# Optimization experiments

Measured on AMD Instinct MI355X. Metric: run time of the kernel, lower is better.

## Reference

```python
import jax, jax.numpy as jnp
import numpy as np

B, TQ, TK, H = 8, 64, 8192, 256


def setup_inputs() -> dict:
    key = jax.random.key(0)
    k1, k2, k3, k4 = jax.random.split(key, 4)
    query = jax.random.normal(k1, (B, TQ, H), dtype=jnp.float32)
    keys = jax.random.normal(k2, (B, TK, H), dtype=jnp.float32)
    # nn.Linear(H, H): weight [H, H], bias [H]; scale like torch default-ish
    Wa_w = jax.random.normal(k3, (H, H), dtype=jnp.float32) * (1.0 / np.sqrt(H))
    Wa_b = jax.random.normal(k4, (H,), dtype=jnp.float32) * 0.01
    return {"query": query, "keys": keys, "Wa_w": Wa_w, "Wa_b": Wa_b}


def reference(query, keys, Wa_w, Wa_b):
    # keys_transformed = keys @ Wa_w.T + Wa_b  (torch Linear semantics)
    keys_t = jnp.einsum('bkh,oh->bko', keys, Wa_w) + Wa_b  # [B,TK,H]
    scores = jnp.einsum('bqh,bkh->bqk', query, keys_t)       # [B,TQ,TK]
    weights = jax.nn.softmax(scores, axis=-1)
    context = jnp.einsum('bqk,bkh->bqh', weights, keys)      # [B,TQ,H]
    return (context, weights)
```

## Files before the change

### kernel.cpp

```cpp
#include <hip/hip_runtime.h>

#define B 8
#define TQ 64
#define TK 8192
#define H 256

#define KSPLIT 32
#define KPB (TK / KSPLIT)
#define CRS 72

typedef __attribute__((ext_vector_type(8))) short bf16x8;
typedef __attribute__((ext_vector_type(4))) float f32x4;
typedef __attribute__((ext_vector_type(4))) unsigned short u16x4;
typedef __attribute__((ext_vector_type(2))) unsigned int u32x2;

static __device__ inline unsigned short f2bf_rne(float x) {
    unsigned int u = __float_as_uint(x);
    unsigned int r = (u + 0x7fffu + ((u >> 16) & 1u)) >> 16;
    return (unsigned short)r;
}

__global__ __launch_bounds__(256) void qtransform_kernel(
    const float* __restrict__ query, const float* __restrict__ Wa_w,
    const float* __restrict__ Wa_b, unsigned short* __restrict__ qthi,
    unsigned short* __restrict__ qtlo, float* __restrict__ qb)
{
    __shared__ float q_s[H];
    __shared__ float red[4];
    const int r = blockIdx.x;
    const int t = threadIdx.x;
    q_s[t] = query[r * H + t];
    __syncthreads();

    float a0 = 0.f, a1 = 0.f, a2 = 0.f, a3 = 0.f;
    for (int o = 0; o < H; o += 4) {
        a0 += q_s[o + 0] * Wa_w[(o + 0) * H + t];
        a1 += q_s[o + 1] * Wa_w[(o + 1) * H + t];
        a2 += q_s[o + 2] * Wa_w[(o + 2) * H + t];
        a3 += q_s[o + 3] * Wa_w[(o + 3) * H + t];
    }
    const float s = (a0 + a1) + (a2 + a3);
    const unsigned int u = __float_as_uint(s);
    const float hif = __uint_as_float(u & 0xFFFF0000u);
    const float lof = s - hif;
    qthi[r * H + t] = (unsigned short)(u >> 16);
    qtlo[r * H + t] = (unsigned short)(__float_as_uint(lof) >> 16);

    float p = q_s[t] * Wa_b[t];
    for (int off = 32; off > 0; off >>= 1) p += __shfl_down(p, off, 64);
    if ((t & 63) == 0) red[t >> 6] = p;
    __syncthreads();
    if (t == 0) qb[r] = (red[0] + red[1]) + (red[2] + red[3]);
}


#define STAGE1(v, row, khb) {                                                  \
    unsigned int u0=__float_as_uint(v.x), u1=__float_as_uint(v.y);             \
    unsigned int u2=__float_as_uint(v.z), u3=__float_as_uint(v.w);             \
    unsigned int h01=(u0>>16)|(u1&0xFFFF0000u), h23=(u2>>16)|(u3&0xFFFF0000u); \
    float l0=v.x-__uint_as_float(u0&0xFFFF0000u);                              \
    float l1=v.y-__uint_as_float(u1&0xFFFF0000u);                              \
    float l2=v.z-__uint_as_float(u2&0xFFFF0000u);                              \
    float l3=v.w-__uint_as_float(u3&0xFFFF0000u);                              \
    unsigned int q01=(__float_as_uint(l0)>>16)|(__float_as_uint(l1)&0xFFFF0000u); \
    unsigned int q23=(__float_as_uint(l2)>>16)|(__float_as_uint(l3)&0xFFFF0000u); \
    int bo=(row)*128 + (((hf>>1)^((row)&7))<<4) + ((hf&1)<<3);                 \
    *(u32x2*)((char*)b_hi+bo) = (u32x2){h01,h23};                              \
    *(u32x2*)((char*)b_lo+bo) = (u32x2){q01,q23};                              \
    *(u32x2*)&khb[(size_t)(row)*H + hf*4] = (u32x2){h01,h23}; }

#define LOADCHUNK(d0,d1,d2,d3, hc)                                             \
    d0 = *(const float4*)&kbase_g[(size_t)(sr +  0) * H + (hc) + hf * 4];      \
    d1 = *(const float4*)&kbase_g[(size_t)(sr + 16) * H + (hc) + hf * 4];      \
    d2 = *(const float4*)&kbase_g[(size_t)(sr + 32) * H + (hc) + hf * 4];      \
    d3 = *(const float4*)&kbase_g[(size_t)(sr + 48) * H + (hc) + hf * 4];

#define STAGECHUNK(v0,v1,v2,v3, hc) {                                          \
    unsigned short* khb = khi_ws + ((size_t)b * TK + k0g) * H + (hc);          \
    STAGE1(v0, sr +  0, khb); STAGE1(v1, sr + 16, khb);                        \
    STAGE1(v2, sr + 32, khb); STAGE1(v3, sr + 48, khb); }

#define COMPUTE(hc) {                                                          \
    _Pragma("unroll")                                                          \
    for (int hs = 0; hs < 64; hs += 32) {                                      \
        bf16x8 ah = *(const bf16x8*)&ah_base[(hc) + hs + lgrp * 8];            \
        bf16x8 al = *(const bf16x8*)&al_base[(hc) + hs + lgrp * 8];            \
        _Pragma("unroll")                                                      \
        for (int nt = 0; nt < 4; ++nt) {                                       \
            int rr = 16 * nt + lrow;                                           \
            int rb = rr * 128 + ((((hs >> 3) + lgrp) ^ (rr & 7)) << 4);        \
            bf16x8 bh = *(const bf16x8*)((const char*)b_hi + rb);              \
            bf16x8 bl = *(const bf16x8*)((const char*)b_lo + rb);              \
            acc[nt] = __builtin_amdgcn_mfma_f32_16x16x32_bf16(ah, bh, acc[nt], 0, 0, 0); \
            acc[nt] = __builtin_amdgcn_mfma_f32_16x16x32_bf16(ah, bl, acc[nt], 0, 0, 0); \
            acc[nt] = __builtin_amdgcn_mfma_f32_16x16x32_bf16(al, bh, acc[nt], 0, 0, 0); \
        } } }

__global__ __launch_bounds__(256, 4) void scores_kernel(
    const unsigned short* __restrict__ qthi, const unsigned short* __restrict__ qtlo,
    const float* __restrict__ qb, const float* __restrict__ keys,
    unsigned short* __restrict__ khi_ws, float* __restrict__ sraw,
    float* __restrict__ pm, float* __restrict__ ps)
{
    __shared__ unsigned short b_hi[64 * 64];
    __shared__ unsigned short b_lo[64 * 64];
    const int t    = threadIdx.x;
    const int kt   = blockIdx.x;
    const int b    = blockIdx.y;
    const int k0g  = kt * 64;
    const int w    = t >> 6;
    const int lane = t & 63;
    const int lrow = lane & 15;
    const int lgrp = lane >> 4;
    const int sr   = t >> 4;
    const int hf   = t & 15;

    const float* kbase_g = keys + (size_t)(b * TK + k0g) * H;
    const unsigned short* ah_base = qthi + (size_t)(b * TQ + 16 * w + lrow) * H;
    const unsigned short* al_base = qtlo + (size_t)(b * TQ + 16 * w + lrow) * H;

    f32x4 acc[4];
    #pragma unroll
    for (int nt = 0; nt < 4; ++nt) acc[nt] = (f32x4){0.f, 0.f, 0.f, 0.f};

    float4 r0, r1, r2, r3, p0, p1, p2, p3;
    LOADCHUNK(r0, r1, r2, r3, 0)

    LOADCHUNK(p0, p1, p2, p3, 64)
    STAGECHUNK(r0, r1, r2, r3, 0)
    __syncthreads();
    COMPUTE(0)
    __syncthreads();

    LOADCHUNK(r0, r1, r2, r3, 128)
    STAGECHUNK(p0, p1, p2, p3, 64)
    __syncthreads();
    COMPUTE(64)
    __syncthreads();

    LOADCHUNK(p0, p1, p2, p3, 192)
    STAGECHUNK(r0, r1, r2, r3, 128)
    __syncthreads();
    COMPUTE(128)
    __syncthreads();

    STAGECHUNK(p0, p1, p2, p3, 192)
    __syncthreads();
    COMPUTE(192)

    #pragma unroll
    for (int j = 0; j < 4; ++j) {
        const int qrow = 16 * w + lgrp * 4 + j;
        const float bias = qb[b * TQ + qrow];
        float v0 = acc[0][j] + bias, v1 = acc[1][j] + bias;
        float v2 = acc[2][j] + bias, v3 = acc[3][j] + bias;
        float* dst = &sraw[(size_t)(b * TQ + qrow) * TK + k0g + lrow];
        dst[0] = v0; dst[16] = v1; dst[32] = v2; dst[48] = v3;
        float m = fmaxf(fmaxf(v0, v1), fmaxf(v2, v3));
        m = fmaxf(m, __shfl_xor(m, 1, 64));
        m = fmaxf(m, __shfl_xor(m, 2, 64));
        m = fmaxf(m, __shfl_xor(m, 4, 64));
        m = fmaxf(m, __shfl_xor(m, 8, 64));
        float e = __expf(v0 - m) + __expf(v1 - m) + __expf(v2 - m) + __expf(v3 - m);
        e += __shfl_xor(e, 1, 64);
        e += __shfl_xor(e, 2, 64);
        e += __shfl_xor(e, 4, 64);
        e += __shfl_xor(e, 8, 64);
        if (lrow == 0) {
            pm[(size_t)(b * TQ + qrow) * 128 + kt] = m;
            ps[(size_t)(b * TQ + qrow) * 128 + kt] = e;
        }
    }
}

__global__ __launch_bounds__(128) void rowreduce_kernel(
    const float* __restrict__ pm, const float* __restrict__ ps,
    float* __restrict__ Mrow, float* __restrict__ Sinv)
{
    const int r = blockIdx.x;
    const int t = threadIdx.x;
    __shared__ float mred[2], sred[2];
    float m = pm[(size_t)r * 128 + t];
    for (int off = 32; off > 0; off >>= 1) m = fmaxf(m, __shfl_xor(m, off, 64));
    if ((t & 63) == 0) mred[t >> 6] = m;
    __syncthreads();
    const float M = fmaxf(mred[0], mred[1]);
    float s = ps[(size_t)r * 128 + t] * __expf(pm[(size_t)r * 128 + t] - M);
    for (int off = 32; off > 0; off >>= 1) s += __shfl_xor(s, off, 64);
    if ((t & 63) == 0) sred[t >> 6] = s;
    __syncthreads();
    if (t == 0) { Mrow[r] = M; Sinv[r] = 1.0f / (sred[0] + sred[1]); }
}

__global__ __launch_bounds__(256) void context_main_kernel(
    const float* __restrict__ sraw, const float* __restrict__ Mrow,
    const float* __restrict__ Sinv, const unsigned short* __restrict__ khi,
    float* __restrict__ part, float* __restrict__ wts)
{
    __shared__ unsigned short kT[64 * CRS];
    const int t    = threadIdx.x;
    const int ks   = blockIdx.x;
    const int ht   = blockIdx.y;
    const int b    = blockIdx.z;
    const int w    = t >> 6;
    const int lane = t & 63;
    const int lrow = lane & 15;
    const int lgrp = lane >> 4;

    const int qrow = b * TQ + 16 * w + lrow;
    const float M  = Mrow[qrow];
    const float Si = Sinv[qrow];

    f32x4 acc[4];
    #pragma unroll
    for (int nt = 0; nt < 4; ++nt) acc[nt] = (f32x4){0.f, 0.f, 0.f, 0.f};

    const int kbase = ks * KPB;
    for (int c = 0; c < KPB; c += 64) {
        __syncthreads();
        #pragma unroll
        for (int i = 0; i < 4; ++i) {
            int idx = t + 256 * i;
            int k = idx >> 4, hq = idx & 15;
            u16x4 v = *(const u16x4*)&khi[((size_t)b * TK + kbase + c + k) * H + ht * 64 + hq * 4];
            #pragma unroll
            for (int c4 = 0; c4 < 4; ++c4) {
                int h = hq * 4 + c4;
                kT[h * CRS + (((k >> 3) ^ ((h >> 3) & 7)) << 3) + (k & 7)] = v[c4];
            }
        }
        __syncthreads();
        #pragma unroll
        for (int kc = 0; kc < 64; kc += 32) {
            const size_t koff = (size_t)qrow * TK + kbase + c + kc + lgrp * 8;
            float4 s0 = *(const float4*)&sraw[koff];
            float4 s1 = *(const float4*)&sraw[koff + 4];
            float p0 = __expf(s0.x - M) * Si, p1 = __expf(s0.y - M) * Si;
            float p2 = __expf(s0.z - M) * Si, p3 = __expf(s0.w - M) * Si;
            float p4 = __expf(s1.x - M) * Si, p5 = __expf(s1.y - M) * Si;
            float p6 = __expf(s1.z - M) * Si, p7 = __expf(s1.w - M) * Si;
            if (ht == 0) {
                *(float4*)&wts[koff] = make_float4(p0, p1, p2, p3);
                *(float4*)&wts[koff + 4] = make_float4(p4, p5, p6, p7);
            }
            u16x4 af0, af1;
            af0[0] = f2bf_rne(p0); af0[1] = f2bf_rne(p1);
            af0[2] = f2bf_rne(p2); af0[3] = f2bf_rne(p3);
            af1[0] = f2bf_rne(p4); af1[1] = f2bf_rne(p5);
            af1[2] = f2bf_rne(p6); af1[3] = f2bf_rne(p7);
            union { u16x4 u[2]; bf16x8 b; } afu;
            afu.u[0] = af0; afu.u[1] = af1;
            #pragma unroll
            for (int nt = 0; nt < 4; ++nt) {
                int h = 16 * nt + lrow;
                bf16x8 bfg = *(const bf16x8*)&kT[h * CRS
                              + ((((kc >> 3) + lgrp) ^ ((h >> 3) & 7)) << 3)];
                acc[nt] = __builtin_amdgcn_mfma_f32_16x16x32_bf16(afu.b, bfg, acc[nt], 0, 0, 0);
            }
        }
    }
    float* dst = part + (size_t)ks * (B * TQ * H);
    #pragma unroll
    for (int j = 0; j < 4; ++j) {
        const int qr = 16 * w + lgrp * 4 + j;
        #pragma unroll
        for (int nt = 0; nt < 4; ++nt)
            dst[(size_t)(b * TQ + qr) * H + ht * 64 + 16 * nt + lrow] = acc[nt][j];
    }
}

__global__ __launch_bounds__(256) void context_reduce_kernel(
    const float* __restrict__ part, float* __restrict__ ctx)
{
    const int idx = blockIdx.x * 256 + threadIdx.x;
    float4 s = make_float4(0.f, 0.f, 0.f, 0.f);
    #pragma unroll 8
    for (int ks = 0; ks < KSPLIT; ++ks) {
        float4 v = *(const float4*)&part[(size_t)ks * (B * TQ * H) + (size_t)idx * 4];
        s.x += v.x; s.y += v.y; s.z += v.z; s.w += v.w;
    }
    *(float4*)&ctx[(size_t)idx * 4] = s;
}

extern "C" void kernel_launch(void* const* d_in, const int* in_sizes, int n_in,
                              void* d_out, int out_size, void* d_ws, size_t ws_size,
                              hipStream_t stream) {
    const float* query = (const float*)d_in[0];
    const float* keys  = (const float*)d_in[1];
    const float* Wa_w  = (const float*)d_in[2];
    const float* Wa_b  = (const float*)d_in[3];

    float* ctx = (float*)d_out;
    float* wts = (float*)d_out + B * TQ * H;

    char* p = (char*)d_ws;
    float* part = (float*)p;                    p += (size_t)KSPLIT * B * TQ * H * 4;
    unsigned short* khi = (unsigned short*)p;   p += (size_t)B * TK * H * 2;
    float* sraw = (float*)p;                    p += (size_t)B * TQ * TK * 4;
    float* pm = (float*)p;                      p += (size_t)B * TQ * 128 * 4;
    float* ps = (float*)p;                      p += (size_t)B * TQ * 128 * 4;
    float* Mr = (float*)p;                      p += (size_t)B * TQ * 4;
    float* Sv = (float*)p;                      p += (size_t)B * TQ * 4;
    unsigned short* qthi = (unsigned short*)p;  p += (size_t)B * TQ * H * 2;
    unsigned short* qtlo = (unsigned short*)p;  p += (size_t)B * TQ * H * 2;
    float* qb = (float*)p;

    qtransform_kernel<<<B * TQ, 256, 0, stream>>>(query, Wa_w, Wa_b, qthi, qtlo, qb);
    scores_kernel<<<dim3(TK / 64, B), 256, 0, stream>>>(qthi, qtlo, qb, keys, khi, sraw, pm, ps);
    rowreduce_kernel<<<B * TQ, 128, 0, stream>>>(pm, ps, Mr, Sv);
    context_main_kernel<<<dim3(KSPLIT, 4, B), 256, 0, stream>>>(sraw, Mr, Sv, khi, part, wts);
    context_reduce_kernel<<<(B * TQ * H / 4) / 256, 256, 0, stream>>>(part, ctx);
}
```

Baseline: 152.9 us.

## Normalize softmax in place in output buffer and feed bf16 probs to context

The scores kernel now writes raw scores straight into the weights output buffer. A new normalize kernel exponentiates and scales them in place and also writes a bf16 copy of the probabilities. The context kernel then reads the compact bf16 copy instead of re-reading fp32 scores four times (once per h-tile) and recomputing exp. This removes redundant exp work and cuts the context kernel's read traffic, at the cost of an extra launch and an extra full pass over the 16 MB weights matrix.

```diff
diff --git a/kernel.cpp b/kernel.cpp
--- a/kernel.cpp
+++ b/kernel.cpp
@@ -99,7 +99,7 @@
 __global__ __launch_bounds__(256, 4) void scores_kernel(
     const unsigned short* __restrict__ qthi, const unsigned short* __restrict__ qtlo,
     const float* __restrict__ qb, const float* __restrict__ keys,
-    unsigned short* __restrict__ khi_ws, float* __restrict__ sraw,
+    unsigned short* __restrict__ khi_ws, float* __restrict__ wraw,
     float* __restrict__ pm, float* __restrict__ ps)
 {
     __shared__ unsigned short b_hi[64 * 64];
@@ -154,7 +154,7 @@
         const float bias = qb[b * TQ + qrow];
         float v0 = acc[0][j] + bias, v1 = acc[1][j] + bias;
         float v2 = acc[2][j] + bias, v3 = acc[3][j] + bias;
-        float* dst = &sraw[(size_t)(b * TQ + qrow) * TK + k0g + lrow];
+        float* dst = &wraw[(size_t)(b * TQ + qrow) * TK + k0g + lrow];
         dst[0] = v0; dst[16] = v1; dst[32] = v2; dst[48] = v3;
         float m = fmaxf(fmaxf(v0, v1), fmaxf(v2, v3));
         m = fmaxf(m, __shfl_xor(m, 1, 64));
@@ -192,10 +192,37 @@
     if (t == 0) { Mrow[r] = M; Sinv[r] = 1.0f / (sred[0] + sred[1]); }
 }
 
+__global__ __launch_bounds__(256) void normalize_kernel(
+    float* __restrict__ wts, const float* __restrict__ Mrow,
+    const float* __restrict__ Sinv, unsigned short* __restrict__ phi)
+{
+    const int r  = blockIdx.y;
+    const int q4 = blockIdx.x;
+    const int t  = threadIdx.x;
+    const float M = Mrow[r], Si = Sinv[r];
+    const size_t base = (size_t)r * TK + q4 * 2048 + t * 8;
+
+    float4 v0 = *(float4*)&wts[base];
+    float4 v1 = *(float4*)&wts[base + 4];
+    v0.x = __expf(v0.x - M) * Si; v0.y = __expf(v0.y - M) * Si;
+    v0.z = __expf(v0.z - M) * Si; v0.w = __expf(v0.w - M) * Si;
+    v1.x = __expf(v1.x - M) * Si; v1.y = __expf(v1.y - M) * Si;
+    v1.z = __expf(v1.z - M) * Si; v1.w = __expf(v1.w - M) * Si;
+    *(float4*)&wts[base] = v0;
+    *(float4*)&wts[base + 4] = v1;
+
+    u16x4 pk0, pk1;
+    pk0[0] = f2bf_rne(v0.x); pk0[1] = f2bf_rne(v0.y);
+    pk0[2] = f2bf_rne(v0.z); pk0[3] = f2bf_rne(v0.w);
+    pk1[0] = f2bf_rne(v1.x); pk1[1] = f2bf_rne(v1.y);
+    pk1[2] = f2bf_rne(v1.z); pk1[3] = f2bf_rne(v1.w);
+    *(u16x4*)&phi[base] = pk0;
+    *(u16x4*)&phi[base + 4] = pk1;
+}
+
 __global__ __launch_bounds__(256) void context_main_kernel(
-    const float* __restrict__ sraw, const float* __restrict__ Mrow,
-    const float* __restrict__ Sinv, const unsigned short* __restrict__ khi,
-    float* __restrict__ part, float* __restrict__ wts)
+    const unsigned short* __restrict__ phi, const unsigned short* __restrict__ khi,
+    float* __restrict__ part)
 {
     __shared__ unsigned short kT[64 * CRS];
     const int t    = threadIdx.x;
@@ -206,10 +233,6 @@
     const int lane = t & 63;
     const int lrow = lane & 15;
     const int lgrp = lane >> 4;
-
-    const int qrow = b * TQ + 16 * w + lrow;
-    const float M  = Mrow[qrow];
-    const float Si = Sinv[qrow];
 
     f32x4 acc[4];
     #pragma unroll
@@ -232,40 +255,24 @@
         __syncthreads();
         #pragma unroll
         for (int kc = 0; kc < 64; kc += 32) {
-            const size_t koff = (size_t)qrow * TK + kbase + c + kc + lgrp * 8;
-            float4 s0 = *(const float4*)&sraw[koff];
-            float4 s1 = *(const float4*)&sraw[koff + 4];
-            float p0 = __expf(s0.x - M) * Si, p1 = __expf(s0.y - M) * Si;
-            float p2 = __expf(s0.z - M) * Si, p3 = __expf(s0.w - M) * Si;
-            float p4 = __expf(s1.x - M) * Si, p5 = __expf(s1.y - M) * Si;
-            float p6 = __expf(s1.z - M) * Si, p7 = __expf(s1.w - M) * Si;
-            if (ht == 0) {
-                *(float4*)&wts[koff] = make_float4(p0, p1, p2, p3);
-                *(float4*)&wts[koff + 4] = make_float4(p4, p5, p6, p7);
-            }
-            u16x4 af0, af1;
-            af0[0] = f2bf_rne(p0); af0[1] = f2bf_rne(p1);
-            af0[2] = f2bf_rne(p2); af0[3] = f2bf_rne(p3);
-            af1[0] = f2bf_rne(p4); af1[1] = f2bf_rne(p5);
-            af1[2] = f2bf_rne(p6); af1[3] = f2bf_rne(p7);
-            union { u16x4 u[2]; bf16x8 b; } afu;
-            afu.u[0] = af0; afu.u[1] = af1;
+            bf16x8 af = *(const bf16x8*)&phi[((size_t)(b * TQ) + 16 * w + lrow) * TK
+                                             + kbase + c + kc + lgrp * 8];
             #pragma unroll
             for (int nt = 0; nt < 4; ++nt) {
                 int h = 16 * nt + lrow;
                 bf16x8 bfg = *(const bf16x8*)&kT[h * CRS
                               + ((((kc >> 3) + lgrp) ^ ((h >> 3) & 7)) << 3)];
-                acc[nt] = __builtin_amdgcn_mfma_f32_16x16x32_bf16(afu.b, bfg, acc[nt], 0, 0, 0);
+                acc[nt] = __builtin_amdgcn_mfma_f32_16x16x32_bf16(af, bfg, acc[nt], 0, 0, 0);
             }
         }
     }
     float* dst = part + (size_t)ks * (B * TQ * H);
     #pragma unroll
     for (int j = 0; j < 4; ++j) {
-        const int qr = 16 * w + lgrp * 4 + j;
+        const int qrow = 16 * w + lgrp * 4 + j;
         #pragma unroll
         for (int nt = 0; nt < 4; ++nt)
-            dst[(size_t)(b * TQ + qr) * H + ht * 64 + 16 * nt + lrow] = acc[nt][j];
+            dst[(size_t)(b * TQ + qrow) * H + ht * 64 + 16 * nt + lrow] = acc[nt][j];
     }
 }
 
@@ -296,7 +303,7 @@
     char* p = (char*)d_ws;
     float* part = (float*)p;                    p += (size_t)KSPLIT * B * TQ * H * 4;
     unsigned short* khi = (unsigned short*)p;   p += (size_t)B * TK * H * 2;
-    float* sraw = (float*)p;                    p += (size_t)B * TQ * TK * 4;
+    unsigned short* phi = (unsigned short*)p;   p += (size_t)B * TQ * TK * 2;
     float* pm = (float*)p;                      p += (size_t)B * TQ * 128 * 4;
     float* ps = (float*)p;                      p += (size_t)B * TQ * 128 * 4;
     float* Mr = (float*)p;                      p += (size_t)B * TQ * 4;
@@ -306,8 +313,9 @@
     float* qb = (float*)p;
 
     qtransform_kernel<<<B * TQ, 256, 0, stream>>>(query, Wa_w, Wa_b, qthi, qtlo, qb);
-    scores_kernel<<<dim3(TK / 64, B), 256, 0, stream>>>(qthi, qtlo, qb, keys, khi, sraw, pm, ps);
+    scores_kernel<<<dim3(TK / 64, B), 256, 0, stream>>>(qthi, qtlo, qb, keys, khi, wts, pm, ps);
     rowreduce_kernel<<<B * TQ, 128, 0, stream>>>(pm, ps, Mr, Sv);
-    context_main_kernel<<<dim3(KSPLIT, 4, B), 256, 0, stream>>>(sraw, Mr, Sv, khi, part, wts);
+    normalize_kernel<<<dim3(4, B * TQ), 256, 0, stream>>>(wts, Mr, Sv, phi);
+    context_main_kernel<<<dim3(KSPLIT, 4, B), 256, 0, stream>>>(phi, khi, part);
     context_reduce_kernel<<<(B * TQ * H / 4) / 256, 256, 0, stream>>>(part, ctx);
 }
```

Measured after the change: 151.4 us. Within noise of the previous version (-1.0%).
